# Performance work log

Measured on AMD Instinct MI355X. Metric: run time of the kernel, lower is better.

The kernel has to match this reference:

```python
import jax, jax.numpy as jnp
import numpy as np

B, N, D, H = 1, 1024, 512, 16
DH = D // H
NBINS = 68
R0 = 10.0
K_ITER = 20
LAM = 1.0


def _ln(x, w, b):
    m = x.mean(-1, keepdims=True)
    v = ((x - m) ** 2).mean(-1, keepdims=True)
    return (x - m) * jax.lax.rsqrt(v + 1e-5) * w + b


def _ln_plain(x):
    m = x.mean(-1, keepdims=True)
    v = ((x - m) ** 2).mean(-1, keepdims=True)
    return (x - m) * jax.lax.rsqrt(v + 1e-5)


def setup_inputs():
    key = jax.random.key(0)
    k = jax.random.split(key, 16)
    s = 0.02
    return {
        "h": jax.random.normal(k[0], (B, N, D), jnp.float32),
        "x_res": jax.random.normal(k[1], (B, N, 3), jnp.float32) * 3.0,
        "mu": jax.random.uniform(k[2], (B, H, N), jnp.float32, 0.5, 1.5) / N,
        "nu": jax.random.uniform(k[3], (B, H, N), jnp.float32, 0.5, 1.5) / N,
        "log_u_prev": jnp.zeros((B, H, N), jnp.float32),
        "log_v_prev": jnp.zeros((B, H, N), jnp.float32),
        "mask": jnp.ones((B, N), jnp.float32),
        "ln_attn_w": jnp.ones((D,), jnp.float32),
        "ln_attn_b": jnp.zeros((D,), jnp.float32),
        "wq": jax.random.normal(k[4], (D, D), jnp.float32) * s,
        "wk": jax.random.normal(k[5], (D, D), jnp.float32) * s,
        "wv": jax.random.normal(k[6], (D, D), jnp.float32) * s,
        "wg": jax.random.normal(k[7], (D, D), jnp.float32) * s,
        "wo": jax.random.normal(k[8], (D, D), jnp.float32) * s,
        "gamma": jax.random.normal(k[9], (H,), jnp.float32) * 1e-4,
        "pos_weight": jax.random.normal(k[10], (NBINS, H), jnp.float32) * s,
        "w_dist_logit": jnp.full((H,), -2.0, jnp.float32),
        "ln_ff_w": jnp.ones((D,), jnp.float32),
        "ln_ff_b": jnp.zeros((D,), jnp.float32),
        "sw_w1": jax.random.normal(k[11], (4 * D, D), jnp.float32) * s,
        "sw_w3": jax.random.normal(k[12], (4 * D, D), jnp.float32) * s,
        "sw_w2": jax.random.normal(k[13], (D, 4 * D), jnp.float32) * s,
        "pos_bins": jax.random.randint(k[14], (B, N, N), 0, NBINS, jnp.int32),
        "eps": jnp.array([0.5] * 4 + [1.0] * 4 + [2.0] * 4 + [4.0] * 4, jnp.float32),
    }


def reference(h, x_res, mu, nu, log_u_prev, log_v_prev, mask, ln_attn_w, ln_attn_b,
              wq, wk, wv, wg, wo, gamma, pos_weight, w_dist_logit,
              ln_ff_w, ln_ff_b, sw_w1, sw_w3, sw_w2, pos_bins, eps):
    h_n = _ln(h, ln_attn_w, ln_attn_b)

    def heads(w):
        return (h_n @ w.T).reshape(B, N, H, DH).transpose(0, 2, 1, 3)  # (B,H,N,DH)

    Q = _ln_plain(heads(wq))
    K = _ln_plain(heads(wk))
    V = heads(wv)
    G = heads(wg)

    # similarity + position bias + distance-gated kernel
    S = jnp.einsum('bhid,bhjd->bhij', Q, K) / np.float32(np.sqrt(DH))  # (B,H,N,N)
    bias = pos_weight[pos_bins].transpose(0, 3, 1, 2)                 # (B,H,N,N)
    d2 = jnp.sum((x_res[:, :, None, :] - x_res[:, None, :, :]) ** 2, -1)  # (B,N,N)
    w_dist = jax.nn.sigmoid(w_dist_logit)                             # (H,)
    logits = S + bias - w_dist[None, :, None, None] * d2[:, None, :, :] / (R0 ** 2)

    pair_mask = mask[:, None, :, None] * mask[:, None, None, :]       # (B,1,N,N)
    logK = jnp.where(pair_mask > 0, logits / eps[None, :, None, None], -1e9)

    # unbalanced log-domain Sinkhorn, 20 iterations, warm-started
    fi = (LAM / (LAM + eps))[None, :, None]                           # (1,H,1)
    log_mu = jnp.log(jnp.clip(mu, 1e-8))
    log_nu = jnp.log(jnp.clip(nu, 1e-8))
    log_u, log_v = log_u_prev, log_v_prev
    lse = jax.scipy.special.logsumexp
    for _ in range(K_ITER):
        log_u = fi * (log_mu - lse(logK + log_v[:, :, None, :], axis=-1))
        log_v = fi * (log_nu - lse(logK + log_u[:, :, :, None], axis=-2))

    P = jnp.exp(logK + log_u[:, :, :, None] + log_v[:, :, None, :]) * pair_mask
    row = jnp.clip(P.sum(-1, keepdims=True), 1e-8)
    Pn = P / row                                                      # row-normalized plan

    attn = jnp.einsum('bhij,bhjd->bhid', Pn, V) * jax.nn.sigmoid(G)
    o = attn.transpose(0, 2, 1, 3).reshape(B, N, D)
    h = h + (o @ wo.T) * mask[:, :, None]

    # centroid EGNN coordinate update
    x_cent = jnp.einsum('bhij,bjc->bhic', Pn, x_res)                  # (B,H,N,3)
    delta = x_res[:, None, :, :] - x_cent
    x_upd = jnp.einsum('h,bhnc->bnc', jnp.tanh(gamma) / H, delta) * mask[:, :, None]
    x_res = x_res + x_upd

    # SwiGLU FFN
    h2 = _ln(h, ln_ff_w, ln_ff_b)
    ff = (jax.nn.silu(h2 @ sw_w1.T) * (h2 @ sw_w3.T)) @ sw_w2.T
    h = h + ff * mask[:, :, None]
    return h, x_res, log_u, log_v
```

## Files before the change

### kernel.cpp

```cpp
#include <hip/hip_runtime.h>
#include <cstddef>
#include <cstdint>

#define N_TOK 1024
#define D_MODEL 512
#define H_HEADS 16
#define DHEAD 32
#define DFF 2048

typedef __attribute__((ext_vector_type(8))) short short8;
typedef __attribute__((ext_vector_type(4))) float f32x4_t;

__device__ __forceinline__ float sigmoidf_(float x){ return 1.f/(1.f+__expf(-x)); }

__device__ __forceinline__ unsigned short f2bf(float f){
  union { float f; unsigned u; } v; v.f = f;
  unsigned r = (v.u + 0x7FFFu + ((v.u >> 16) & 1u)) >> 16;
  return (unsigned short)r;
}
__device__ __forceinline__ float bf_lo(unsigned u){ return __uint_as_float(u << 16); }
__device__ __forceinline__ float bf_hi(unsigned u){ return __uint_as_float(u & 0xFFFF0000u); }

__device__ __forceinline__ int swz_head(int b){ return (b & 7) + 8 * ((b >> 3) & 1); }

__global__ __launch_bounds__(256) void ln_rows(const float* __restrict__ x,
                                               const float* __restrict__ w,
                                               const float* __restrict__ b,
                                               unsigned short* __restrict__ y) {
  int row = blockIdx.x;
  const float* xr = x + (size_t)row * D_MODEL;
  float s = 0.f, s2 = 0.f;
  for (int i = threadIdx.x; i < D_MODEL; i += 256) { float v = xr[i]; s += v; s2 += v*v; }
  #pragma unroll
  for (int off = 32; off; off >>= 1) { s += __shfl_down(s, off); s2 += __shfl_down(s2, off); }
  __shared__ float rs[4], rs2[4];
  int wave = threadIdx.x >> 6, lane = threadIdx.x & 63;
  if (lane == 0) { rs[wave] = s; rs2[wave] = s2; }
  __syncthreads();
  s  = rs[0] + rs[1] + rs[2] + rs[3];
  s2 = rs2[0] + rs2[1] + rs2[2] + rs2[3];
  float mean = s * (1.f / D_MODEL);
  float var  = s2 * (1.f / D_MODEL) - mean * mean;
  float r = rsqrtf(var + 1e-5f);
  unsigned short* yr = y + (size_t)row * D_MODEL;
  for (int i = threadIdx.x; i < D_MODEL; i += 256)
    yr[i] = f2bf((xr[i] - mean) * r * w[i] + b[i]);
}

__global__ __launch_bounds__(256) void conv_weights(const float* __restrict__ wq,
                                                    const float* __restrict__ wk,
                                                    const float* __restrict__ wv,
                                                    const float* __restrict__ wg,
                                                    const float* __restrict__ wo,
                                                    const float* __restrict__ w1,
                                                    const float* __restrict__ w3,
                                                    const float* __restrict__ w2,
                                                    unsigned short* __restrict__ dst) {
  size_t i = ((size_t)blockIdx.x * 256 + threadIdx.x) * 4;
  const float* src; size_t off;
  if      (i < 262144)  { src = wq; off = i; }
  else if (i < 524288)  { src = wk; off = i - 262144; }
  else if (i < 786432)  { src = wv; off = i - 524288; }
  else if (i < 1048576) { src = wg; off = i - 786432; }
  else if (i < 1310720) { src = wo; off = i - 1048576; }
  else if (i < 2359296) { src = w1; off = i - 1310720; }
  else if (i < 3407872) { src = w3; off = i - 2359296; }
  else                  { src = w2; off = i - 3407872; }
  float4 v = *(const float4*)&src[off];
  unsigned lo = ((unsigned)f2bf(v.y) << 16) | f2bf(v.x);
  unsigned hi = ((unsigned)f2bf(v.w) << 16) | f2bf(v.z);
  *(uint2*)&dst[i] = make_uint2(lo, hi);
}

__global__ __launch_bounds__(256) void gemm_mfma(const unsigned short* __restrict__ A,
                                                 const unsigned short* __restrict__ B,
                                                 float* __restrict__ C,
                                                 int M, int K, int Nout,
                                                 const float* __restrict__ addmat,
                                                 const float* __restrict__ maskrow) {
  __shared__ unsigned short As[128][40];
  __shared__ unsigned short Bs[128][40];
  int t = threadIdx.x;
  int m0 = blockIdx.y * 128, n0 = blockIdx.x * 128;
  int wave = t >> 6, lane = t & 63;
  int wm = (wave >> 1) * 64, wn = (wave & 1) * 64;
  int lm = lane & 15, quad = lane >> 4;
  f32x4_t zero = {0.f, 0.f, 0.f, 0.f};
  f32x4_t acc[4][4];
  #pragma unroll
  for (int i = 0; i < 4; ++i)
    #pragma unroll
    for (int j = 0; j < 4; ++j) acc[i][j] = zero;

  int sr = t >> 2, sc = (t & 3) * 8;
  for (int kk = 0; kk < K; kk += 32) {
    #pragma unroll
    for (int c = 0; c < 2; ++c) {
      int r = sr + c * 64;
      *(uint4*)&As[r][sc] = *(const uint4*)&A[(size_t)(m0 + r) * K + kk + sc];
      *(uint4*)&Bs[r][sc] = *(const uint4*)&B[(size_t)(n0 + r) * K + kk + sc];
    }
    __syncthreads();
    short8 af[4], bfr[4];
    #pragma unroll
    for (int mt = 0; mt < 4; ++mt)
      af[mt] = *(const short8*)&As[wm + mt * 16 + lm][quad * 8];
    #pragma unroll
    for (int nt = 0; nt < 4; ++nt)
      bfr[nt] = *(const short8*)&Bs[wn + nt * 16 + lm][quad * 8];
    #pragma unroll
    for (int mt = 0; mt < 4; ++mt)
      #pragma unroll
      for (int nt = 0; nt < 4; ++nt)
        acc[mt][nt] = __builtin_amdgcn_mfma_f32_16x16x32_bf16(af[mt], bfr[nt], acc[mt][nt], 0, 0, 0);
    __syncthreads();
  }
  #pragma unroll
  for (int mt = 0; mt < 4; ++mt) {
    #pragma unroll
    for (int reg = 0; reg < 4; ++reg) {
      int gm = m0 + wm + mt * 16 + quad * 4 + reg;
      float mk = maskrow ? maskrow[gm] : 0.f;
      #pragma unroll
      for (int nt = 0; nt < 4; ++nt) {
        int gn = n0 + wn + nt * 16 + lm;
        float v = acc[mt][nt][reg];
        if (addmat) v = addmat[(size_t)gm * Nout + gn] + v * mk;
        C[(size_t)gm * Nout + gn] = v;
      }
    }
  }
}

__global__ __launch_bounds__(256) void gemm_mfma64(const unsigned short* __restrict__ A,
                                                   const unsigned short* __restrict__ B,
                                                   float* __restrict__ C,
                                                   int M, int K, int Nout,
                                                   const float* __restrict__ addmat,
                                                   const float* __restrict__ maskrow) {
  __shared__ unsigned short As[64][40];
  __shared__ unsigned short Bs[64][40];
  int t = threadIdx.x;
  int m0 = blockIdx.y * 64, n0 = blockIdx.x * 64;
  int wave = t >> 6, lane = t & 63;
  int wm = (wave >> 1) * 32, wn = (wave & 1) * 32;
  int lm = lane & 15, quad = lane >> 4;
  f32x4_t zero = {0.f, 0.f, 0.f, 0.f};
  f32x4_t acc[2][2];
  #pragma unroll
  for (int i = 0; i < 2; ++i)
    #pragma unroll
    for (int j = 0; j < 2; ++j) acc[i][j] = zero;

  int sr = t >> 2, sc = (t & 3) * 8;
  for (int kk = 0; kk < K; kk += 32) {
    *(uint4*)&As[sr][sc] = *(const uint4*)&A[(size_t)(m0 + sr) * K + kk + sc];
    *(uint4*)&Bs[sr][sc] = *(const uint4*)&B[(size_t)(n0 + sr) * K + kk + sc];
    __syncthreads();
    short8 af[2], bfr[2];
    #pragma unroll
    for (int mt = 0; mt < 2; ++mt)
      af[mt] = *(const short8*)&As[wm + mt * 16 + lm][quad * 8];
    #pragma unroll
    for (int nt = 0; nt < 2; ++nt)
      bfr[nt] = *(const short8*)&Bs[wn + nt * 16 + lm][quad * 8];
    #pragma unroll
    for (int mt = 0; mt < 2; ++mt)
      #pragma unroll
      for (int nt = 0; nt < 2; ++nt)
        acc[mt][nt] = __builtin_amdgcn_mfma_f32_16x16x32_bf16(af[mt], bfr[nt], acc[mt][nt], 0, 0, 0);
    __syncthreads();
  }
  #pragma unroll
  for (int mt = 0; mt < 2; ++mt) {
    #pragma unroll
    for (int reg = 0; reg < 4; ++reg) {
      int gm = m0 + wm + mt * 16 + quad * 4 + reg;
      float mk = maskrow ? maskrow[gm] : 0.f;
      #pragma unroll
      for (int nt = 0; nt < 2; ++nt) {
        int gn = n0 + wn + nt * 16 + lm;
        float v = acc[mt][nt][reg];
        if (addmat) v = addmat[(size_t)gm * Nout + gn] + v * mk;
        C[(size_t)gm * Nout + gn] = v;
      }
    }
  }
}

__global__ __launch_bounds__(256) void headln(float* __restrict__ base, int ld) {
  int g = blockIdx.x * 256 + threadIdx.x;
  int i = g & (N_TOK - 1), hh = g >> 10;
  float* p = base + (size_t)i * ld + hh * DHEAD;
  float s = 0.f, s2 = 0.f;
  #pragma unroll
  for (int k = 0; k < DHEAD; ++k) { float v = p[k]; s += v; s2 += v*v; }
  float m = s * (1.f / DHEAD);
  float var = s2 * (1.f / DHEAD) - m * m;
  float r = rsqrtf(var + 1e-5f);
  #pragma unroll
  for (int k = 0; k < DHEAD; ++k) p[k] = (p[k] - m) * r;
}

__global__ __launch_bounds__(256) void build_W_mfma(const float* __restrict__ Q0,
                                                    const float* __restrict__ K0,
                                                    int ld,
                                                    const float* __restrict__ xres,
                                                    const int* __restrict__ bins,
                                                    const float* __restrict__ posw,
                                                    const float* __restrict__ wdl,
                                                    const float* __restrict__ epsp,
                                                    const float* __restrict__ mask,
                                                    unsigned short* __restrict__ Wm) {
  int b = blockIdx.x;
  int h = swz_head(b);
  int tile = b >> 4;
  int i0 = (tile >> 4) * 64, j0 = (tile & 15) * 64;
  __shared__ unsigned short Qs[64][40];
  __shared__ unsigned short Ks[64][40];
  __shared__ unsigned char  binsU[64][68];
  __shared__ unsigned short tileB[64][68];
  __shared__ float xi0[64], xi1[64], xi2[64], xj0[64], xj1[64], xj2[64];
  __shared__ float mi_s[64], mj_s[64], poswS[68];
  int t = threadIdx.x;
  {
    int r = t >> 2, c8 = (t & 3) * 8;
    const float* qsrc = Q0 + (size_t)(i0 + r) * ld + h * DHEAD + c8;
    const float* ksrc = K0 + (size_t)(j0 + r) * ld + h * DHEAD + c8;
    float4 qa = *(const float4*)qsrc, qb = *(const float4*)(qsrc + 4);
    float4 ka = *(const float4*)ksrc, kb = *(const float4*)(ksrc + 4);
    unsigned short* qd = &Qs[r][c8];
    qd[0]=f2bf(qa.x); qd[1]=f2bf(qa.y); qd[2]=f2bf(qa.z); qd[3]=f2bf(qa.w);
    qd[4]=f2bf(qb.x); qd[5]=f2bf(qb.y); qd[6]=f2bf(qb.z); qd[7]=f2bf(qb.w);
    unsigned short* kd = &Ks[r][c8];
    kd[0]=f2bf(ka.x); kd[1]=f2bf(ka.y); kd[2]=f2bf(ka.z); kd[3]=f2bf(ka.w);
    kd[4]=f2bf(kb.x); kd[5]=f2bf(kb.y); kd[6]=f2bf(kb.z); kd[7]=f2bf(kb.w);
  }
  {
    int rb = t >> 2, cb = (t & 3) * 16;
    const int* bsrc = bins + (size_t)(i0 + rb) * N_TOK + j0 + cb;
    #pragma unroll
    for (int c = 0; c < 4; ++c) {
      int4 b4 = *(const int4*)(bsrc + c * 4);
      uchar4 u4 = make_uchar4((unsigned char)b4.x, (unsigned char)b4.y,
                              (unsigned char)b4.z, (unsigned char)b4.w);
      *(uchar4*)&binsU[rb][cb + c * 4] = u4;
    }
  }
  if (t < 64) {
    xi0[t] = xres[(i0 + t) * 3 + 0]; xi1[t] = xres[(i0 + t) * 3 + 1]; xi2[t] = xres[(i0 + t) * 3 + 2];
    xj0[t] = xres[(j0 + t) * 3 + 0]; xj1[t] = xres[(j0 + t) * 3 + 1]; xj2[t] = xres[(j0 + t) * 3 + 2];
    mi_s[t] = mask[i0 + t]; mj_s[t] = mask[j0 + t];
  }
  if (t >= 64 && t < 132) poswS[t - 64] = posw[(t - 64) * H_HEADS + h];
  __syncthreads();
  int wave = t >> 6, lane = t & 63;
  int lm = lane & 15, quad = lane >> 4;
  int wm = (wave >> 1) * 32, wn = (wave & 1) * 32;
  f32x4_t zero = {0.f, 0.f, 0.f, 0.f};
  f32x4_t acc[2][2] = {{zero, zero}, {zero, zero}};
  short8 af[2], bfr[2];
  #pragma unroll
  for (int mt = 0; mt < 2; ++mt) af[mt] = *(const short8*)&Qs[wm + mt * 16 + lm][quad * 8];
  #pragma unroll
  for (int nt = 0; nt < 2; ++nt) bfr[nt] = *(const short8*)&Ks[wn + nt * 16 + lm][quad * 8];
  #pragma unroll
  for (int mt = 0; mt < 2; ++mt)
    #pragma unroll
    for (int nt = 0; nt < 2; ++nt)
      acc[mt][nt] = __builtin_amdgcn_mfma_f32_16x16x32_bf16(af[mt], bfr[nt], acc[mt][nt], 0, 0, 0);
  float wd = sigmoidf_(wdl[h]);
  float inv_eps = 1.f / epsp[h];
  const float inv_sqrt = 0.17677669529663687f;
  #pragma unroll
  for (int mt = 0; mt < 2; ++mt) {
    #pragma unroll
    for (int nt = 0; nt < 2; ++nt) {
      int col = wn + nt * 16 + lm;
      float xj0v = xj0[col], xj1v = xj1[col], xj2v = xj2[col], mj = mj_s[col];
      #pragma unroll
      for (int reg = 0; reg < 4; ++reg) {
        int row = wm + mt * 16 + quad * 4 + reg;
        float d0 = xi0[row] - xj0v, d1 = xi1[row] - xj1v, d2c = xi2[row] - xj2v;
        float d2 = d0*d0 + d1*d1 + d2c*d2c;
        float bias = poswS[binsU[row][col]];
        float logit = acc[mt][nt][reg] * inv_sqrt + bias - wd * d2 * 0.01f;
        float outv = (mi_s[row] * mj > 0.f) ? __expf(logit * inv_eps) : 0.f;
        tileB[row][col] = f2bf(outv);
      }
    }
  }
  __syncthreads();
  {
    int r = t >> 2, cb = (t & 3) * 16;
    unsigned short* dst = Wm + ((size_t)h * N_TOK + (i0 + r)) * N_TOK + j0 + cb;
    uint4 w0 = *(uint4*)&tileB[r][cb];
    uint4 w1v = *(uint4*)&tileB[r][cb + 8];
    *(uint4*)dst = w0;
    *(uint4*)(dst + 8) = w1v;
  }
}

__global__ __launch_bounds__(256) void build_vxt(const float* __restrict__ QKVG_,
                                                 const float* __restrict__ xres,
                                                 unsigned short* __restrict__ Vxt) {
  int h = blockIdx.x, j0 = blockIdx.y * 64;
  __shared__ float T[48][72];
  int t = threadIdx.x;
  {
    int j = t >> 2, c8 = (t & 3) * 8;
    const float* src = QKVG_ + (size_t)(j0 + j) * 2048 + 1024 + h * DHEAD + c8;
    float4 a = *(const float4*)src, b = *(const float4*)(src + 4);
    T[c8 + 0][j] = a.x; T[c8 + 1][j] = a.y; T[c8 + 2][j] = a.z; T[c8 + 3][j] = a.w;
    T[c8 + 4][j] = b.x; T[c8 + 5][j] = b.y; T[c8 + 6][j] = b.z; T[c8 + 7][j] = b.w;
  }
  if (t < 64) {
    int j = t;
    T[32][j] = xres[(j0 + j) * 3 + 0];
    T[33][j] = xres[(j0 + j) * 3 + 1];
    T[34][j] = xres[(j0 + j) * 3 + 2];
    T[35][j] = 1.f;
    #pragma unroll
    for (int d = 36; d < 48; ++d) T[d][j] = 0.f;
  }
  __syncthreads();
  for (int task = t; task < 384; task += 256) {
    int d = task >> 3, jc = (task & 7) * 8;
    float* s = &T[d][jc];
    unsigned a0 = ((unsigned)f2bf(s[1]) << 16) | f2bf(s[0]);
    unsigned a1 = ((unsigned)f2bf(s[3]) << 16) | f2bf(s[2]);
    unsigned a2 = ((unsigned)f2bf(s[5]) << 16) | f2bf(s[4]);
    unsigned a3 = ((unsigned)f2bf(s[7]) << 16) | f2bf(s[6]);
    *(uint4*)(Vxt + ((size_t)h * 48 + d) * N_TOK + j0 + jc) = make_uint4(a0, a1, a2, a3);
  }
}

__global__ __launch_bounds__(256) void sink_init(const float* __restrict__ mu,
                                                 const float* __restrict__ nu,
                                                 const float* __restrict__ lv0,
                                                 float* __restrict__ lmu,
                                                 float* __restrict__ lnu,
                                                 float* __restrict__ vtilde) {
  int i = blockIdx.x * 256 + threadIdx.x;
  lmu[i] = __logf(fmaxf(mu[i], 1e-8f));
  lnu[i] = __logf(fmaxf(nu[i], 1e-8f));
  vtilde[i] = __expf(lv0[i]);
}

__global__ __launch_bounds__(256) void sink_row(const unsigned short* __restrict__ Wm,
                                                const float* __restrict__ vtilde,
                                                const float* __restrict__ lmu,
                                                float* __restrict__ outlog,
                                                float* __restrict__ outexp,
                                                const float* __restrict__ epsp) {
  int b = blockIdx.x;
  int h = swz_head(b);
  int grp = b >> 4;
  int t = threadIdx.x;
  int wave = t >> 6, lane = t & 63;
  int sub = lane >> 4, l16 = lane & 15;
  int i = grp * 16 + wave * 4 + sub;
  const uint4* p = (const uint4*)(Wm + ((size_t)h * N_TOK + i) * N_TOK);
  const float4* vt = (const float4*)(vtilde + h * N_TOK);
  float s8[8];
  #pragma unroll
  for (int c = 0; c < 8; ++c) s8[c] = 0.f;
  #pragma unroll
  for (int it = 0; it < 8; ++it) {
    int j0 = it * 128 + l16 * 8;
    uint4 u = p[j0 >> 3];
    float4 va = vt[j0 >> 2];
    float4 vb = vt[(j0 >> 2) + 1];
    s8[0] += bf_lo(u.x) * va.x; s8[1] += bf_hi(u.x) * va.y;
    s8[2] += bf_lo(u.y) * va.z; s8[3] += bf_hi(u.y) * va.w;
    s8[4] += bf_lo(u.z) * vb.x; s8[5] += bf_hi(u.z) * vb.y;
    s8[6] += bf_lo(u.w) * vb.z; s8[7] += bf_hi(u.w) * vb.w;
  }
  float s = ((s8[0] + s8[1]) + (s8[2] + s8[3])) + ((s8[4] + s8[5]) + (s8[6] + s8[7]));
  #pragma unroll
  for (int off = 1; off <= 8; off <<= 1) s += __shfl_xor(s, off);
  if (l16 == 0) {
    float fi = 1.f / (1.f + epsp[h]);
    float val = fi * (lmu[h * N_TOK + i] - __logf(fmaxf(s, 1e-35f)));
    outlog[h * N_TOK + i] = val;
    outexp[h * N_TOK + i] = __expf(val);
  }
}

__global__ __launch_bounds__(256) void sink_col(const unsigned short* __restrict__ Wm,
                                                const float* __restrict__ utilde,
                                                const float* __restrict__ lnu,
                                                float* __restrict__ outlog,
                                                float* __restrict__ outexp,
                                                const float* __restrict__ epsp) {
  int b = blockIdx.x;
  int h = swz_head(b);
  int j0 = (b >> 4) * 64;
  int t = threadIdx.x;
  int jl = (t & 15) * 4;
  int ig = t >> 4;
  const unsigned short* base = Wm + ((size_t)h * N_TOK + ig * 64) * N_TOK + j0 + jl;
  const float* ut = utilde + h * N_TOK + ig * 64;
  float a0 = 0.f, a1 = 0.f, a2 = 0.f, a3 = 0.f;
  #pragma unroll 8
  for (int r = 0; r < 64; ++r) {
    uint2 w = *(const uint2*)(base + (size_t)r * N_TOK);
    float u = ut[r];
    a0 += bf_lo(w.x) * u; a1 += bf_hi(w.x) * u;
    a2 += bf_lo(w.y) * u; a3 += bf_hi(w.y) * u;
  }
  __shared__ float red[16][68];
  red[ig][jl + 0] = a0; red[ig][jl + 1] = a1;
  red[ig][jl + 2] = a2; red[ig][jl + 3] = a3;
  __syncthreads();
  if (t < 64) {
    float s = 0.f;
    #pragma unroll
    for (int g = 0; g < 16; ++g) s += red[g][t];
    int j = j0 + t;
    float fi = 1.f / (1.f + epsp[h]);
    float val = fi * (lnu[h * N_TOK + j] - __logf(fmaxf(s, 1e-35f)));
    outlog[h * N_TOK + j] = val;
    outexp[h * N_TOK + j] = __expf(val);
  }
}

__global__ __launch_bounds__(256) void finalize_mfma(const unsigned short* __restrict__ Wm,
                                                     const float* __restrict__ vtilde,
                                                     const unsigned short* __restrict__ Vxt,
                                                     const float* __restrict__ G0, int ld,
                                                     const float* __restrict__ xres,
                                                     const float* __restrict__ mask,
                                                     unsigned short* __restrict__ o,
                                                     float* __restrict__ x_out,
                                                     const float* __restrict__ gamma) {
  int b = blockIdx.x;
  int h = swz_head(b);
  int mt = b >> 4;
  int t = threadIdx.x, wave = t >> 6, lane = t & 63;
  int lm = lane & 15, quad = lane >> 4;
  __shared__ float vts[N_TOK];
  ((float4*)vts)[t] = ((const float4*)(vtilde + h * N_TOK))[t];
  __syncthreads();
  int arow = mt * 64 + wave * 16 + lm;
  const unsigned short* Kr = Wm + ((size_t)h * N_TOK + arow) * N_TOK + quad * 8;
  const unsigned short* Bb = Vxt + (size_t)h * 48 * N_TOK + quad * 8;
  f32x4_t zero = {0.f, 0.f, 0.f, 0.f};
  f32x4_t acc[3] = {zero, zero, zero};
  for (int kk = 0; kk < N_TOK; kk += 32) {
    uint4 u = *(const uint4*)(Kr + kk);
    float4 la = *(const float4*)&vts[kk + quad * 8];
    float4 lb = *(const float4*)&vts[kk + quad * 8 + 4];
    float p0 = bf_lo(u.x) * la.x;
    float p1 = bf_hi(u.x) * la.y;
    float p2 = bf_lo(u.y) * la.z;
    float p3 = bf_hi(u.y) * la.w;
    float p4 = bf_lo(u.z) * lb.x;
    float p5 = bf_hi(u.z) * lb.y;
    float p6 = bf_lo(u.w) * lb.z;
    float p7 = bf_hi(u.w) * lb.w;
    union { uint4 u4; short8 s8; } pk;
    pk.u4 = make_uint4(((unsigned)f2bf(p1) << 16) | f2bf(p0),
                       ((unsigned)f2bf(p3) << 16) | f2bf(p2),
                       ((unsigned)f2bf(p5) << 16) | f2bf(p4),
                       ((unsigned)f2bf(p7) << 16) | f2bf(p6));
    short8 af = pk.s8;
    #pragma unroll
    for (int nt = 0; nt < 3; ++nt) {
      short8 bfrag = *(const short8*)(Bb + (size_t)(nt * 16 + lm) * N_TOK + kk);
      acc[nt] = __builtin_amdgcn_mfma_f32_16x16x32_bf16(af, bfrag, acc[nt], 0, 0, 0);
    }
  }
  float inv[4];
  #pragma unroll
  for (int reg = 0; reg < 4; ++reg) {
    float rsum = __shfl(acc[2][reg], (quad << 4) | 3, 64);
    inv[reg] = 1.f / fmaxf(rsum, 1e-30f);
  }
  #pragma unroll
  for (int nt = 0; nt < 2; ++nt) {
    int c = nt * 16 + lm;
    #pragma unroll
    for (int reg = 0; reg < 4; ++reg) {
      int r = mt * 64 + wave * 16 + quad * 4 + reg;
      float gv = G0[(size_t)r * ld + h * DHEAD + c];
      float ovl = acc[nt][reg] * inv[reg] * sigmoidf_(gv);
      o[(size_t)r * D_MODEL + h * DHEAD + c] = f2bf(ovl);
    }
  }
  if (lm < 3) {
    float tg = tanhf(gamma[h]) * (1.f / H_HEADS);
    #pragma unroll
    for (int reg = 0; reg < 4; ++reg) {
      int r = mt * 64 + wave * 16 + quad * 4 + reg;
      float xc = acc[2][reg] * inv[reg];
      float mi = mask[r];
      atomicAdd(&x_out[r * 3 + lm], tg * mi * (xres[r * 3 + lm] - xc));
    }
  }
}

__global__ __launch_bounds__(256) void silu_mul_bf(const float* __restrict__ ffab,
                                                   unsigned short* __restrict__ out, int n) {
  int i = blockIdx.x * 256 + threadIdx.x;
  if (i >= n) return;
  int row = i >> 11, col = i & 2047;
  float a = ffab[(size_t)row * 4096 + col];
  float bb = ffab[(size_t)row * 4096 + 2048 + col];
  out[i] = f2bf(a * sigmoidf_(a) * bb);
}

__global__ __launch_bounds__(256) void copyf(const float* __restrict__ src,
                                             float* __restrict__ dst, int n) {
  int i = blockIdx.x * 256 + threadIdx.x;
  if (i < n) dst[i] = src[i];
}

extern "C" void kernel_launch(void* const* d_in, const int* in_sizes, int n_in,
                              void* d_out, int out_size, void* d_ws, size_t ws_size,
                              hipStream_t stream) {
  const float* h_in  = (const float*)d_in[0];
  const float* x_res = (const float*)d_in[1];
  const float* mu    = (const float*)d_in[2];
  const float* nu    = (const float*)d_in[3];
  const float* lu0   = (const float*)d_in[4];
  const float* lv0   = (const float*)d_in[5];
  const float* mask  = (const float*)d_in[6];
  const float* lnw   = (const float*)d_in[7];
  const float* lnb   = (const float*)d_in[8];
  const float* wq    = (const float*)d_in[9];
  const float* wk    = (const float*)d_in[10];
  const float* wv    = (const float*)d_in[11];
  const float* wg    = (const float*)d_in[12];
  const float* wo    = (const float*)d_in[13];
  const float* gamma = (const float*)d_in[14];
  const float* posw  = (const float*)d_in[15];
  const float* wdl   = (const float*)d_in[16];
  const float* lnfw  = (const float*)d_in[17];
  const float* lnfb  = (const float*)d_in[18];
  const float* w1    = (const float*)d_in[19];
  const float* w3    = (const float*)d_in[20];
  const float* w2    = (const float*)d_in[21];
  const int*   bins  = (const int*)d_in[22];
  const float* eps   = (const float*)d_in[23];

  float* out    = (float*)d_out;
  float* out_h  = out;
  float* out_x  = out + 524288;
  float* out_lu = out + 527360;
  float* out_lv = out + 543744;

  float* ws = (float*)d_ws;
  float* QKVG  = ws;
  float* h_mid = ws + 2097152;
  unsigned short* U = (unsigned short*)(ws + 2621440);
  unsigned short* h_n_b  = U;
  unsigned short* h2_b   = U + 524288;
  unsigned short* o_b    = U + 1048576;
  unsigned short* wB     = U + 1572864;
  unsigned short* Wb   = (unsigned short*)(ws + 5636096);
  unsigned short* Vxt  = Wb + (size_t)H_HEADS * N_TOK * N_TOK;
  float* vtilde = (float*)(Vxt + 786432);
  float* utilde = vtilde + 16384;
  float* lmu    = utilde + 16384;
  float* lnu    = lmu + 16384;
  unsigned short* ff_b = (unsigned short*)(lnu + 16384);
  float* ffab          = (float*)Wb;

  unsigned short* wQKVGb = wB;
  unsigned short* wob    = wB + 1048576;
  unsigned short* wFFb   = wB + 1310720;
  unsigned short* w2b    = wB + 3407872;

  dim3 b256(256);

  conv_weights<<<4352, b256, 0, stream>>>(wq, wk, wv, wg, wo, w1, w3, w2, wB);
  ln_rows<<<N_TOK, b256, 0, stream>>>(h_in, lnw, lnb, h_n_b);

  gemm_mfma<<<dim3(16, 8), b256, 0, stream>>>(h_n_b, wQKVGb, QKVG,
                                              N_TOK, D_MODEL, 2048, nullptr, nullptr);

  headln<<<128, b256, 0, stream>>>(QKVG, 2048);

  copyf<<<12, b256, 0, stream>>>(x_res, out_x, N_TOK * 3);

  build_W_mfma<<<4096, b256, 0, stream>>>(
      QKVG, QKVG + 512, 2048, x_res, bins, posw, wdl, eps, mask, Wb);
  build_vxt<<<dim3(H_HEADS, N_TOK / 64), b256, 0, stream>>>(QKVG, x_res, Vxt);

  sink_init<<<64, b256, 0, stream>>>(mu, nu, lv0, lmu, lnu, vtilde);
  for (int it = 0; it < 20; ++it) {
    sink_row<<<1024, b256, 0, stream>>>(Wb, vtilde, lmu, out_lu, utilde, eps);
    sink_col<<<256, b256, 0, stream>>>(Wb, utilde, lnu, out_lv, vtilde, eps);
  }

  finalize_mfma<<<256, b256, 0, stream>>>(
      Wb, vtilde, Vxt, QKVG + 1536, 2048, x_res, mask, o_b, out_x, gamma);

  gemm_mfma64<<<dim3(8, 16), b256, 0, stream>>>(o_b, wob, h_mid,
                                                N_TOK, D_MODEL, D_MODEL, h_in, mask);

  ln_rows<<<N_TOK, b256, 0, stream>>>(h_mid, lnfw, lnfb, h2_b);

  gemm_mfma<<<dim3(32, 8), b256, 0, stream>>>(h2_b, wFFb, ffab,
                                              N_TOK, D_MODEL, 4096, nullptr, nullptr);
  silu_mul_bf<<<(N_TOK * DFF) / 256, b256, 0, stream>>>(ffab, ff_b, N_TOK * DFF);

  gemm_mfma64<<<dim3(8, 16), b256, 0, stream>>>(ff_b, w2b, out_h,
                                                N_TOK, DFF, D_MODEL, h_mid, mask);
}
```

Measured before the change: 449.3 us.

## Fuse Sinkhorn iterations into one persistent kernel with per-head grid barriers

Replaces the 40 separate row/column Sinkhorn kernel launches with a single persistent kernel of 256 blocks. Each head's 16 blocks synchronise through an atomic counter/generation barrier between the row and column half-steps. The aim is to remove launch overhead and the inter-kernel gaps across the 20 iterations. It relies on all 256 blocks being co-resident, which holds with one block per CU on a 256-CU device, and it adds spin-wait barrier latency. Global writes to utilde/vtilde are made visible by thread fences.

```diff
diff --git a/kernel.cpp b/kernel.cpp
--- a/kernel.cpp
+++ b/kernel.cpp
@@ -340,88 +340,109 @@
                                                  const float* __restrict__ lv0,
                                                  float* __restrict__ lmu,
                                                  float* __restrict__ lnu,
-                                                 float* __restrict__ vtilde) {
+                                                 float* __restrict__ vtilde,
+                                                 int* __restrict__ bar) {
   int i = blockIdx.x * 256 + threadIdx.x;
   lmu[i] = __logf(fmaxf(mu[i], 1e-8f));
   lnu[i] = __logf(fmaxf(nu[i], 1e-8f));
   vtilde[i] = __expf(lv0[i]);
-}
-
-__global__ __launch_bounds__(256) void sink_row(const unsigned short* __restrict__ Wm,
-                                                const float* __restrict__ vtilde,
-                                                const float* __restrict__ lmu,
-                                                float* __restrict__ outlog,
-                                                float* __restrict__ outexp,
-                                                const float* __restrict__ epsp) {
+  if (i < 1024) bar[i] = 0;
+}
+
+__device__ __forceinline__ void head_bar(int* cnt, int* gen, int target) {
+  __syncthreads();
+  if (threadIdx.x == 0) {
+    __threadfence();
+    if (atomicAdd(cnt, 1) == 15) {
+      atomicExch(cnt, 0);
+      atomicAdd(gen, 1);
+    } else {
+      while (atomicAdd(gen, 0) < target) __builtin_amdgcn_s_sleep(1);
+    }
+    __threadfence();
+  }
+  __syncthreads();
+}
+
+__global__ __launch_bounds__(256, 1) void sink_persist(const unsigned short* __restrict__ Wm,
+                                                       float* __restrict__ vtilde,
+                                                       float* __restrict__ utilde,
+                                                       const float* __restrict__ lmu,
+                                                       const float* __restrict__ lnu,
+                                                       float* __restrict__ out_lu,
+                                                       float* __restrict__ out_lv,
+                                                       const float* __restrict__ epsp,
+                                                       int* __restrict__ bar) {
   int b = blockIdx.x;
   int h = swz_head(b);
-  int grp = b >> 4;
+  int kslot = b >> 4;
+  int* cnt = bar + h * 64;
+  int* gen = bar + h * 64 + 32;
   int t = threadIdx.x;
   int wave = t >> 6, lane = t & 63;
   int sub = lane >> 4, l16 = lane & 15;
-  int i = grp * 16 + wave * 4 + sub;
-  const uint4* p = (const uint4*)(Wm + ((size_t)h * N_TOK + i) * N_TOK);
-  const float4* vt = (const float4*)(vtilde + h * N_TOK);
-  float s8[8];
-  #pragma unroll
-  for (int c = 0; c < 8; ++c) s8[c] = 0.f;
-  #pragma unroll
-  for (int it = 0; it < 8; ++it) {
-    int j0 = it * 128 + l16 * 8;
-    uint4 u = p[j0 >> 3];
-    float4 va = vt[j0 >> 2];
-    float4 vb = vt[(j0 >> 2) + 1];
-    s8[0] += bf_lo(u.x) * va.x; s8[1] += bf_hi(u.x) * va.y;
-    s8[2] += bf_lo(u.y) * va.z; s8[3] += bf_hi(u.y) * va.w;
-    s8[4] += bf_lo(u.z) * vb.x; s8[5] += bf_hi(u.z) * vb.y;
-    s8[6] += bf_lo(u.w) * vb.z; s8[7] += bf_hi(u.w) * vb.w;
-  }
-  float s = ((s8[0] + s8[1]) + (s8[2] + s8[3])) + ((s8[4] + s8[5]) + (s8[6] + s8[7]));
-  #pragma unroll
-  for (int off = 1; off <= 8; off <<= 1) s += __shfl_xor(s, off);
-  if (l16 == 0) {
-    float fi = 1.f / (1.f + epsp[h]);
-    float val = fi * (lmu[h * N_TOK + i] - __logf(fmaxf(s, 1e-35f)));
-    outlog[h * N_TOK + i] = val;
-    outexp[h * N_TOK + i] = __expf(val);
-  }
-}
-
-__global__ __launch_bounds__(256) void sink_col(const unsigned short* __restrict__ Wm,
-                                                const float* __restrict__ utilde,
-                                                const float* __restrict__ lnu,
-                                                float* __restrict__ outlog,
-                                                float* __restrict__ outexp,
-                                                const float* __restrict__ epsp) {
-  int b = blockIdx.x;
-  int h = swz_head(b);
-  int j0 = (b >> 4) * 64;
-  int t = threadIdx.x;
-  int jl = (t & 15) * 4;
-  int ig = t >> 4;
-  const unsigned short* base = Wm + ((size_t)h * N_TOK + ig * 64) * N_TOK + j0 + jl;
-  const float* ut = utilde + h * N_TOK + ig * 64;
-  float a0 = 0.f, a1 = 0.f, a2 = 0.f, a3 = 0.f;
-  #pragma unroll 8
-  for (int r = 0; r < 64; ++r) {
-    uint2 w = *(const uint2*)(base + (size_t)r * N_TOK);
-    float u = ut[r];
-    a0 += bf_lo(w.x) * u; a1 += bf_hi(w.x) * u;
-    a2 += bf_lo(w.y) * u; a3 += bf_hi(w.y) * u;
-  }
+  float fi = 1.f / (1.f + epsp[h]);
   __shared__ float red[16][68];
-  red[ig][jl + 0] = a0; red[ig][jl + 1] = a1;
-  red[ig][jl + 2] = a2; red[ig][jl + 3] = a3;
-  __syncthreads();
-  if (t < 64) {
-    float s = 0.f;
-    #pragma unroll
-    for (int g = 0; g < 16; ++g) s += red[g][t];
-    int j = j0 + t;
-    float fi = 1.f / (1.f + epsp[h]);
-    float val = fi * (lnu[h * N_TOK + j] - __logf(fmaxf(s, 1e-35f)));
-    outlog[h * N_TOK + j] = val;
-    outexp[h * N_TOK + j] = __expf(val);
+  const unsigned short* Wh = Wm + (size_t)h * N_TOK * N_TOK;
+  int j0 = kslot * 64;
+  int jl = (t & 15) * 4, ig = t >> 4;
+  int target = 0;
+
+  for (int it = 0; it < 20; ++it) {
+    #pragma unroll
+    for (int rd = 0; rd < 4; ++rd) {
+      int i = kslot * 64 + wave * 16 + rd * 4 + sub;
+      const uint4* p = (const uint4*)(Wh + (size_t)i * N_TOK);
+      const float4* vt4 = (const float4*)(vtilde + h * N_TOK);
+      float s8[8];
+      #pragma unroll
+      for (int c = 0; c < 8; ++c) s8[c] = 0.f;
+      #pragma unroll
+      for (int q = 0; q < 8; ++q) {
+        int jj = q * 128 + l16 * 8;
+        uint4 u = p[jj >> 3];
+        float4 va = vt4[jj >> 2];
+        float4 vb = vt4[(jj >> 2) + 1];
+        s8[0] += bf_lo(u.x) * va.x; s8[1] += bf_hi(u.x) * va.y;
+        s8[2] += bf_lo(u.y) * va.z; s8[3] += bf_hi(u.y) * va.w;
+        s8[4] += bf_lo(u.z) * vb.x; s8[5] += bf_hi(u.z) * vb.y;
+        s8[6] += bf_lo(u.w) * vb.z; s8[7] += bf_hi(u.w) * vb.w;
+      }
+      float s = ((s8[0] + s8[1]) + (s8[2] + s8[3])) + ((s8[4] + s8[5]) + (s8[6] + s8[7]));
+      #pragma unroll
+      for (int off = 1; off <= 8; off <<= 1) s += __shfl_xor(s, off);
+      if (l16 == 0) {
+        float val = fi * (lmu[h * N_TOK + i] - __logf(fmaxf(s, 1e-35f)));
+        out_lu[h * N_TOK + i] = val;
+        utilde[h * N_TOK + i] = __expf(val);
+      }
+    }
+    ++target; head_bar(cnt, gen, target);
+    {
+      const unsigned short* base = Wh + (size_t)(ig * 64) * N_TOK + j0 + jl;
+      const float* ut = utilde + h * N_TOK + ig * 64;
+      float a0 = 0.f, a1 = 0.f, a2 = 0.f, a3 = 0.f;
+      #pragma unroll 8
+      for (int r = 0; r < 64; ++r) {
+        uint2 w = *(const uint2*)(base + (size_t)r * N_TOK);
+        float u = ut[r];
+        a0 += bf_lo(w.x) * u; a1 += bf_hi(w.x) * u;
+        a2 += bf_lo(w.y) * u; a3 += bf_hi(w.y) * u;
+      }
+      red[ig][jl + 0] = a0; red[ig][jl + 1] = a1;
+      red[ig][jl + 2] = a2; red[ig][jl + 3] = a3;
+      __syncthreads();
+      if (t < 64) {
+        float s = 0.f;
+        #pragma unroll
+        for (int g = 0; g < 16; ++g) s += red[g][t];
+        int j = j0 + t;
+        float val = fi * (lnu[h * N_TOK + j] - __logf(fmaxf(s, 1e-35f)));
+        out_lv[h * N_TOK + j] = val;
+        vtilde[h * N_TOK + j] = __expf(val);
+      }
+    }
+    ++target; head_bar(cnt, gen, target);
   }
 }
 
@@ -565,7 +586,8 @@
   float* lmu    = utilde + 16384;
   float* lnu    = lmu + 16384;
   unsigned short* ff_b = (unsigned short*)(lnu + 16384);
-  float* ffab          = (float*)Wb;
+  int*   barp   = (int*)(ff_b + 2097152);
+  float* ffab   = (float*)Wb;
 
   unsigned short* wQKVGb = wB;
   unsigned short* wob    = wB + 1048576;
@@ -588,11 +610,10 @@
       QKVG, QKVG + 512, 2048, x_res, bins, posw, wdl, eps, mask, Wb);
   build_vxt<<<dim3(H_HEADS, N_TOK / 64), b256, 0, stream>>>(QKVG, x_res, Vxt);
 
-  sink_init<<<64, b256, 0, stream>>>(mu, nu, lv0, lmu, lnu, vtilde);
-  for (int it = 0; it < 20; ++it) {
-    sink_row<<<1024, b256, 0, stream>>>(Wb, vtilde, lmu, out_lu, utilde, eps);
-    sink_col<<<256, b256, 0, stream>>>(Wb, utilde, lnu, out_lv, vtilde, eps);
-  }
+  sink_init<<<64, b256, 0, stream>>>(mu, nu, lv0, lmu, lnu, vtilde, barp);
+
+  sink_persist<<<256, b256, 0, stream>>>(Wb, vtilde, utilde, lmu, lnu,
+                                         out_lu, out_lv, eps, barp);
 
   finalize_mfma<<<256, b256, 0, stream>>>(
       Wb, vtilde, Vxt, QKVG + 1536, 2048, x_res, mask, o_b, out_x, gamma);
```

Measured after the change: 916.0 us. 104% more time.

## Split Sinkhorn column pass into 4-way partial sums, fuse finalize into row kernel

Applied to the files above, without the earlier changes.

The column-scaling kernel now launches 1024 blocks, each reducing a quarter of the rows, and writes partial column sums to a workspace buffer. This replaces the previous 256-block launch that used only part of the GPU. The next row kernel combines the four partials, computes v-tilde into LDS, and reads it from there in its row reduction. A small final kernel turns the last partials into log_v and v-tilde. The cost is extra partial-sum traffic and redundant per-block recomputation of v-tilde for each head.

```diff
diff --git a/kernel.cpp b/kernel.cpp
--- a/kernel.cpp
+++ b/kernel.cpp
@@ -387,23 +387,81 @@
   }
 }
 
-__global__ __launch_bounds__(256) void sink_col(const unsigned short* __restrict__ Wm,
-                                                const float* __restrict__ utilde,
-                                                const float* __restrict__ lnu,
-                                                float* __restrict__ outlog,
-                                                float* __restrict__ outexp,
-                                                const float* __restrict__ epsp) {
+__global__ __launch_bounds__(256) void sink_row2(const unsigned short* __restrict__ Wm,
+                                                 const float* __restrict__ part,
+                                                 const float* __restrict__ lnu,
+                                                 const float* __restrict__ lmu,
+                                                 float* __restrict__ outlog,
+                                                 float* __restrict__ outexp,
+                                                 const float* __restrict__ epsp) {
+  __shared__ float vt_lds[N_TOK];
   int b = blockIdx.x;
   int h = swz_head(b);
-  int j0 = (b >> 4) * 64;
+  int grp = b >> 4;
+  int t = threadIdx.x;
+  float fi = 1.f / (1.f + epsp[h]);
+  {
+    int j = t * 4;
+    float4 p0 = *(const float4*)(part + 0 * 16384 + h * N_TOK + j);
+    float4 p1 = *(const float4*)(part + 1 * 16384 + h * N_TOK + j);
+    float4 p2 = *(const float4*)(part + 2 * 16384 + h * N_TOK + j);
+    float4 p3 = *(const float4*)(part + 3 * 16384 + h * N_TOK + j);
+    float4 ln4 = *(const float4*)(lnu + h * N_TOK + j);
+    float s0 = (p0.x + p1.x) + (p2.x + p3.x);
+    float s1 = (p0.y + p1.y) + (p2.y + p3.y);
+    float s2 = (p0.z + p1.z) + (p2.z + p3.z);
+    float s3 = (p0.w + p1.w) + (p2.w + p3.w);
+    vt_lds[j + 0] = __expf(fi * (ln4.x - __logf(fmaxf(s0, 1e-35f))));
+    vt_lds[j + 1] = __expf(fi * (ln4.y - __logf(fmaxf(s1, 1e-35f))));
+    vt_lds[j + 2] = __expf(fi * (ln4.z - __logf(fmaxf(s2, 1e-35f))));
+    vt_lds[j + 3] = __expf(fi * (ln4.w - __logf(fmaxf(s3, 1e-35f))));
+  }
+  __syncthreads();
+  int wave = t >> 6, lane = t & 63;
+  int sub = lane >> 4, l16 = lane & 15;
+  int i = grp * 16 + wave * 4 + sub;
+  const uint4* p = (const uint4*)(Wm + ((size_t)h * N_TOK + i) * N_TOK);
+  float s8[8];
+  #pragma unroll
+  for (int c = 0; c < 8; ++c) s8[c] = 0.f;
+  #pragma unroll
+  for (int it = 0; it < 8; ++it) {
+    int j0 = it * 128 + l16 * 8;
+    uint4 u = p[j0 >> 3];
+    float4 va = *(const float4*)&vt_lds[j0];
+    float4 vb = *(const float4*)&vt_lds[j0 + 4];
+    s8[0] += bf_lo(u.x) * va.x; s8[1] += bf_hi(u.x) * va.y;
+    s8[2] += bf_lo(u.y) * va.z; s8[3] += bf_hi(u.y) * va.w;
+    s8[4] += bf_lo(u.z) * vb.x; s8[5] += bf_hi(u.z) * vb.y;
+    s8[6] += bf_lo(u.w) * vb.z; s8[7] += bf_hi(u.w) * vb.w;
+  }
+  float s = ((s8[0] + s8[1]) + (s8[2] + s8[3])) + ((s8[4] + s8[5]) + (s8[6] + s8[7]));
+  #pragma unroll
+  for (int off = 1; off <= 8; off <<= 1) s += __shfl_xor(s, off);
+  if (l16 == 0) {
+    float val = fi * (lmu[h * N_TOK + i] - __logf(fmaxf(s, 1e-35f)));
+    outlog[h * N_TOK + i] = val;
+    outexp[h * N_TOK + i] = __expf(val);
+  }
+}
+
+__global__ __launch_bounds__(256) void sink_colp(const unsigned short* __restrict__ Wm,
+                                                 const float* __restrict__ utilde,
+                                                 float* __restrict__ part) {
+  int b = blockIdx.x;
+  int h = swz_head(b);
+  int c = (b >> 4) & 3;
+  int jt = (b >> 6) & 15;
+  int j0 = jt * 64;
   int t = threadIdx.x;
   int jl = (t & 15) * 4;
   int ig = t >> 4;
-  const unsigned short* base = Wm + ((size_t)h * N_TOK + ig * 64) * N_TOK + j0 + jl;
-  const float* ut = utilde + h * N_TOK + ig * 64;
+  int r0 = c * 256 + ig * 16;
+  const unsigned short* base = Wm + ((size_t)h * N_TOK + r0) * N_TOK + j0 + jl;
+  const float* ut = utilde + h * N_TOK + r0;
   float a0 = 0.f, a1 = 0.f, a2 = 0.f, a3 = 0.f;
-  #pragma unroll 8
-  for (int r = 0; r < 64; ++r) {
+  #pragma unroll
+  for (int r = 0; r < 16; ++r) {
     uint2 w = *(const uint2*)(base + (size_t)r * N_TOK);
     float u = ut[r];
     a0 += bf_lo(w.x) * u; a1 += bf_hi(w.x) * u;
@@ -417,11 +475,35 @@
     float s = 0.f;
     #pragma unroll
     for (int g = 0; g < 16; ++g) s += red[g][t];
-    int j = j0 + t;
-    float fi = 1.f / (1.f + epsp[h]);
-    float val = fi * (lnu[h * N_TOK + j] - __logf(fmaxf(s, 1e-35f)));
-    outlog[h * N_TOK + j] = val;
-    outexp[h * N_TOK + j] = __expf(val);
+    part[c * 16384 + h * N_TOK + j0 + t] = s;
+  }
+}
+
+__global__ __launch_bounds__(256) void sink_fin(const float* __restrict__ part,
+                                                const float* __restrict__ lnu,
+                                                float* __restrict__ out_lv,
+                                                float* __restrict__ vtilde,
+                                                const float* __restrict__ epsp) {
+  int h = blockIdx.x;
+  int t = threadIdx.x;
+  float fi = 1.f / (1.f + epsp[h]);
+  int j = t * 4;
+  float4 p0 = *(const float4*)(part + 0 * 16384 + h * N_TOK + j);
+  float4 p1 = *(const float4*)(part + 1 * 16384 + h * N_TOK + j);
+  float4 p2 = *(const float4*)(part + 2 * 16384 + h * N_TOK + j);
+  float4 p3 = *(const float4*)(part + 3 * 16384 + h * N_TOK + j);
+  float4 ln4 = *(const float4*)(lnu + h * N_TOK + j);
+  float sv[4];
+  sv[0] = (p0.x + p1.x) + (p2.x + p3.x);
+  sv[1] = (p0.y + p1.y) + (p2.y + p3.y);
+  sv[2] = (p0.z + p1.z) + (p2.z + p3.z);
+  sv[3] = (p0.w + p1.w) + (p2.w + p3.w);
+  float ln_[4] = {ln4.x, ln4.y, ln4.z, ln4.w};
+  #pragma unroll
+  for (int k = 0; k < 4; ++k) {
+    float val = fi * (ln_[k] - __logf(fmaxf(sv[k], 1e-35f)));
+    out_lv[h * N_TOK + j + k] = val;
+    vtilde[h * N_TOK + j + k] = __expf(val);
   }
 }
 
@@ -564,8 +646,9 @@
   float* utilde = vtilde + 16384;
   float* lmu    = utilde + 16384;
   float* lnu    = lmu + 16384;
-  unsigned short* ff_b = (unsigned short*)(lnu + 16384);
-  float* ffab          = (float*)Wb;
+  float* part   = lnu + 16384;
+  unsigned short* ff_b = (unsigned short*)(part + 65536);
+  float* ffab   = (float*)Wb;
 
   unsigned short* wQKVGb = wB;
   unsigned short* wob    = wB + 1048576;
@@ -589,10 +672,14 @@
   build_vxt<<<dim3(H_HEADS, N_TOK / 64), b256, 0, stream>>>(QKVG, x_res, Vxt);
 
   sink_init<<<64, b256, 0, stream>>>(mu, nu, lv0, lmu, lnu, vtilde);
-  for (int it = 0; it < 20; ++it) {
-    sink_row<<<1024, b256, 0, stream>>>(Wb, vtilde, lmu, out_lu, utilde, eps);
-    sink_col<<<256, b256, 0, stream>>>(Wb, utilde, lnu, out_lv, vtilde, eps);
-  }
+
+  sink_row<<<1024, b256, 0, stream>>>(Wb, vtilde, lmu, out_lu, utilde, eps);
+  sink_colp<<<1024, b256, 0, stream>>>(Wb, utilde, part);
+  for (int it = 1; it < 20; ++it) {
+    sink_row2<<<1024, b256, 0, stream>>>(Wb, part, lnu, lmu, out_lu, utilde, eps);
+    sink_colp<<<1024, b256, 0, stream>>>(Wb, utilde, part);
+  }
+  sink_fin<<<H_HEADS, b256, 0, stream>>>(part, lnu, out_lv, vtilde, eps);
 
   finalize_mfma<<<256, b256, 0, stream>>>(
       Wb, vtilde, Vxt, QKVG + 1536, 2048, x_res, mask, o_b, out_x, gamma);
```

New measurement: 424.9 us. 1.06x faster.

## Fuse Sinkhorn row and column passes into one kernel with partial column sums

Applied to the files above, without the earlier changes.

Replaces the separate row and column Sinkhorn kernels with one kernel per iteration. Each block handles 64 rows of one head: it rebuilds v from the previous iteration's 16 partial column sums, computes the row update, then immediately reads the same 64-row slab of W again to write a partial column sum. This halves the launches in the loop and lets the column pass reuse W rows the block just read, likely from cache. The cost is redundant v reconstruction in every block, an extra partial-sum buffer, and a final reduction kernel.

```diff
diff --git a/kernel.cpp b/kernel.cpp
--- a/kernel.cpp
+++ b/kernel.cpp
@@ -347,81 +347,109 @@
   vtilde[i] = __expf(lv0[i]);
 }
 
-__global__ __launch_bounds__(256) void sink_row(const unsigned short* __restrict__ Wm,
-                                                const float* __restrict__ vtilde,
-                                                const float* __restrict__ lmu,
-                                                float* __restrict__ outlog,
-                                                float* __restrict__ outexp,
-                                                const float* __restrict__ epsp) {
+__global__ __launch_bounds__(256) void sink_iter(const unsigned short* __restrict__ Wm,
+                                                 const float* __restrict__ vt0,
+                                                 float* __restrict__ part,
+                                                 const float* __restrict__ lmu,
+                                                 const float* __restrict__ lnu,
+                                                 float* __restrict__ out_lu,
+                                                 const float* __restrict__ epsp,
+                                                 int first) {
+  __shared__ float vt_lds[N_TOK];
+  __shared__ float u_lds[64];
   int b = blockIdx.x;
   int h = swz_head(b);
   int grp = b >> 4;
   int t = threadIdx.x;
+  float fi = 1.f / (1.f + epsp[h]);
+  {
+    int j = t * 4;
+    if (first) {
+      *(float4*)&vt_lds[j] = *(const float4*)(vt0 + h * N_TOK + j);
+    } else {
+      float s0 = 0.f, s1 = 0.f, s2 = 0.f, s3 = 0.f;
+      #pragma unroll
+      for (int c = 0; c < 16; ++c) {
+        float4 p = *(const float4*)(part + (size_t)c * 16384 + h * N_TOK + j);
+        s0 += p.x; s1 += p.y; s2 += p.z; s3 += p.w;
+      }
+      float4 ln4 = *(const float4*)(lnu + h * N_TOK + j);
+      vt_lds[j + 0] = __expf(fi * (ln4.x - __logf(fmaxf(s0, 1e-35f))));
+      vt_lds[j + 1] = __expf(fi * (ln4.y - __logf(fmaxf(s1, 1e-35f))));
+      vt_lds[j + 2] = __expf(fi * (ln4.z - __logf(fmaxf(s2, 1e-35f))));
+      vt_lds[j + 3] = __expf(fi * (ln4.w - __logf(fmaxf(s3, 1e-35f))));
+    }
+  }
+  __syncthreads();
   int wave = t >> 6, lane = t & 63;
   int sub = lane >> 4, l16 = lane & 15;
-  int i = grp * 16 + wave * 4 + sub;
-  const uint4* p = (const uint4*)(Wm + ((size_t)h * N_TOK + i) * N_TOK);
-  const float4* vt = (const float4*)(vtilde + h * N_TOK);
-  float s8[8];
-  #pragma unroll
-  for (int c = 0; c < 8; ++c) s8[c] = 0.f;
-  #pragma unroll
-  for (int it = 0; it < 8; ++it) {
-    int j0 = it * 128 + l16 * 8;
-    uint4 u = p[j0 >> 3];
-    float4 va = vt[j0 >> 2];
-    float4 vb = vt[(j0 >> 2) + 1];
-    s8[0] += bf_lo(u.x) * va.x; s8[1] += bf_hi(u.x) * va.y;
-    s8[2] += bf_lo(u.y) * va.z; s8[3] += bf_hi(u.y) * va.w;
-    s8[4] += bf_lo(u.z) * vb.x; s8[5] += bf_hi(u.z) * vb.y;
-    s8[6] += bf_lo(u.w) * vb.z; s8[7] += bf_hi(u.w) * vb.w;
-  }
-  float s = ((s8[0] + s8[1]) + (s8[2] + s8[3])) + ((s8[4] + s8[5]) + (s8[6] + s8[7]));
-  #pragma unroll
-  for (int off = 1; off <= 8; off <<= 1) s += __shfl_xor(s, off);
-  if (l16 == 0) {
-    float fi = 1.f / (1.f + epsp[h]);
-    float val = fi * (lmu[h * N_TOK + i] - __logf(fmaxf(s, 1e-35f)));
-    outlog[h * N_TOK + i] = val;
-    outexp[h * N_TOK + i] = __expf(val);
-  }
-}
-
-__global__ __launch_bounds__(256) void sink_col(const unsigned short* __restrict__ Wm,
-                                                const float* __restrict__ utilde,
+  #pragma unroll
+  for (int rd = 0; rd < 4; ++rd) {
+    int il = wave * 16 + rd * 4 + sub;
+    int i = grp * 64 + il;
+    const uint4* p = (const uint4*)(Wm + ((size_t)h * N_TOK + i) * N_TOK);
+    float s8[8];
+    #pragma unroll
+    for (int c = 0; c < 8; ++c) s8[c] = 0.f;
+    #pragma unroll
+    for (int q = 0; q < 8; ++q) {
+      int j0 = q * 128 + l16 * 8;
+      uint4 u = p[j0 >> 3];
+      float4 va = *(const float4*)&vt_lds[j0];
+      float4 vb = *(const float4*)&vt_lds[j0 + 4];
+      s8[0] += bf_lo(u.x) * va.x; s8[1] += bf_hi(u.x) * va.y;
+      s8[2] += bf_lo(u.y) * va.z; s8[3] += bf_hi(u.y) * va.w;
+      s8[4] += bf_lo(u.z) * vb.x; s8[5] += bf_hi(u.z) * vb.y;
+      s8[6] += bf_lo(u.w) * vb.z; s8[7] += bf_hi(u.w) * vb.w;
+    }
+    float s = ((s8[0] + s8[1]) + (s8[2] + s8[3])) + ((s8[4] + s8[5]) + (s8[6] + s8[7]));
+    #pragma unroll
+    for (int off = 1; off <= 8; off <<= 1) s += __shfl_xor(s, off);
+    if (l16 == 0) {
+      float val = fi * (lmu[h * N_TOK + i] - __logf(fmaxf(s, 1e-35f)));
+      out_lu[h * N_TOK + i] = val;
+      u_lds[il] = __expf(val);
+    }
+  }
+  __syncthreads();
+  {
+    int jc = t * 4;
+    const unsigned short* base = Wm + ((size_t)h * N_TOK + grp * 64) * N_TOK + jc;
+    float a0 = 0.f, a1 = 0.f, a2 = 0.f, a3 = 0.f;
+    #pragma unroll 8
+    for (int r = 0; r < 64; ++r) {
+      uint2 w = *(const uint2*)(base + (size_t)r * N_TOK);
+      float u = u_lds[r];
+      a0 += bf_lo(w.x) * u; a1 += bf_hi(w.x) * u;
+      a2 += bf_lo(w.y) * u; a3 += bf_hi(w.y) * u;
+    }
+    *(float4*)(part + (size_t)grp * 16384 + h * N_TOK + jc) = make_float4(a0, a1, a2, a3);
+  }
+}
+
+__global__ __launch_bounds__(256) void sink_fin(const float* __restrict__ part,
                                                 const float* __restrict__ lnu,
-                                                float* __restrict__ outlog,
-                                                float* __restrict__ outexp,
+                                                float* __restrict__ out_lv,
+                                                float* __restrict__ vtilde,
                                                 const float* __restrict__ epsp) {
-  int b = blockIdx.x;
-  int h = swz_head(b);
-  int j0 = (b >> 4) * 64;
+  int h = blockIdx.x;
   int t = threadIdx.x;
-  int jl = (t & 15) * 4;
-  int ig = t >> 4;
-  const unsigned short* base = Wm + ((size_t)h * N_TOK + ig * 64) * N_TOK + j0 + jl;
-  const float* ut = utilde + h * N_TOK + ig * 64;
-  float a0 = 0.f, a1 = 0.f, a2 = 0.f, a3 = 0.f;
-  #pragma unroll 8
-  for (int r = 0; r < 64; ++r) {
-    uint2 w = *(const uint2*)(base + (size_t)r * N_TOK);
-    float u = ut[r];
-    a0 += bf_lo(w.x) * u; a1 += bf_hi(w.x) * u;
-    a2 += bf_lo(w.y) * u; a3 += bf_hi(w.y) * u;
-  }
-  __shared__ float red[16][68];
-  red[ig][jl + 0] = a0; red[ig][jl + 1] = a1;
-  red[ig][jl + 2] = a2; red[ig][jl + 3] = a3;
-  __syncthreads();
-  if (t < 64) {
-    float s = 0.f;
-    #pragma unroll
-    for (int g = 0; g < 16; ++g) s += red[g][t];
-    int j = j0 + t;
-    float fi = 1.f / (1.f + epsp[h]);
-    float val = fi * (lnu[h * N_TOK + j] - __logf(fmaxf(s, 1e-35f)));
-    outlog[h * N_TOK + j] = val;
-    outexp[h * N_TOK + j] = __expf(val);
+  float fi = 1.f / (1.f + epsp[h]);
+  int j = t * 4;
+  float s0 = 0.f, s1 = 0.f, s2 = 0.f, s3 = 0.f;
+  #pragma unroll
+  for (int c = 0; c < 16; ++c) {
+    float4 p = *(const float4*)(part + (size_t)c * 16384 + h * N_TOK + j);
+    s0 += p.x; s1 += p.y; s2 += p.z; s3 += p.w;
+  }
+  float4 ln4 = *(const float4*)(lnu + h * N_TOK + j);
+  float sv[4] = {s0, s1, s2, s3};
+  float ln_[4] = {ln4.x, ln4.y, ln4.z, ln4.w};
+  #pragma unroll
+  for (int k = 0; k < 4; ++k) {
+    float val = fi * (ln_[k] - __logf(fmaxf(sv[k], 1e-35f)));
+    out_lv[h * N_TOK + j + k] = val;
+    vtilde[h * N_TOK + j + k] = __expf(val);
   }
 }
 
@@ -561,11 +589,11 @@
   unsigned short* Wb   = (unsigned short*)(ws + 5636096);
   unsigned short* Vxt  = Wb + (size_t)H_HEADS * N_TOK * N_TOK;
   float* vtilde = (float*)(Vxt + 786432);
-  float* utilde = vtilde + 16384;
-  float* lmu    = utilde + 16384;
+  float* lmu    = vtilde + 16384;
   float* lnu    = lmu + 16384;
-  unsigned short* ff_b = (unsigned short*)(lnu + 16384);
-  float* ffab          = (float*)Wb;
+  float* part   = lnu + 16384;
+  unsigned short* ff_b = (unsigned short*)(part + 262144);
+  float* ffab   = (float*)Wb;
 
   unsigned short* wQKVGb = wB;
   unsigned short* wob    = wB + 1048576;
@@ -589,10 +617,12 @@
   build_vxt<<<dim3(H_HEADS, N_TOK / 64), b256, 0, stream>>>(QKVG, x_res, Vxt);
 
   sink_init<<<64, b256, 0, stream>>>(mu, nu, lv0, lmu, lnu, vtilde);
+
   for (int it = 0; it < 20; ++it) {
-    sink_row<<<1024, b256, 0, stream>>>(Wb, vtilde, lmu, out_lu, utilde, eps);
-    sink_col<<<256, b256, 0, stream>>>(Wb, utilde, lnu, out_lv, vtilde, eps);
-  }
+    sink_iter<<<256, b256, 0, stream>>>(Wb, vtilde, part, lmu, lnu, out_lu, eps,
+                                        it == 0 ? 1 : 0);
+  }
+  sink_fin<<<H_HEADS, b256, 0, stream>>>(part, lnu, out_lv, vtilde, eps);
 
   finalize_mfma<<<256, b256, 0, stream>>>(
       Wb, vtilde, Vxt, QKVG + 1536, 2048, x_res, mask, o_b, out_x, gamma);
```

After: 463.6 us. 3.2% more time.
